# Performance work log

Measured on AMD Instinct MI355X. Metric: run time of the kernel, lower is better.

Reference implementation:

```python
import jax, jax.numpy as jnp
import numpy as np

B, T, D, H, DFF, E = 4, 1024, 1024, 16, 4096, 8
DH = D // H
EPS = 1e-6


def setup_inputs() -> dict:
    key = jax.random.key(0)
    ks = jax.random.split(key, 16)
    s = 0.02
    return {
        "x": jax.random.normal(ks[0], (B, T, D), jnp.float32),
        "mask": jnp.ones((B, 1, 1, T), jnp.bool_),
        "Wq": jax.random.normal(ks[1], (D, D), jnp.float32) * s,
        "bq": jnp.zeros((D,), jnp.float32),
        "Wk": jax.random.normal(ks[2], (D, D), jnp.float32) * s,
        "bk": jnp.zeros((D,), jnp.float32),
        "Wv": jax.random.normal(ks[3], (D, D), jnp.float32) * s,
        "bv": jnp.zeros((D,), jnp.float32),
        "Wo": jax.random.normal(ks[4], (D, D), jnp.float32) * s,
        "bo": jnp.zeros((D,), jnp.float32),
        "ln1_a": jnp.ones((D,), jnp.float32),
        "ln1_b": jnp.zeros((D,), jnp.float32),
        "ln2_a": jnp.ones((D,), jnp.float32),
        "ln2_b": jnp.zeros((D,), jnp.float32),
        "gW": jax.random.normal(ks[5], (D, E), jnp.float32) * s,
        "gb": jnp.zeros((E,), jnp.float32),
        "W1": jax.random.normal(ks[6], (E, D, DFF), jnp.float32) * s,
        "b1": jnp.zeros((E, DFF), jnp.float32),
        "W2": jax.random.normal(ks[7], (E, DFF, D), jnp.float32) * s,
        "b2": jnp.zeros((E, D), jnp.float32),
    }


def layer_norm(x, a, b):
    # Faithful to source: torch std is unbiased (ddof=1), divides by (std + eps)
    mean = jnp.mean(x, -1, keepdims=True)
    std = jnp.std(x, -1, keepdims=True, ddof=1)
    return a * (x - mean) / (std + EPS) + b


def mha(x, mask, Wq, bq, Wk, bk, Wv, bv, Wo, bo):
    def split(h):
        return h.reshape(B, T, H, DH).transpose(0, 2, 1, 3)  # [B,H,T,DH]
    q = split(x @ Wq + bq)
    k = split(x @ Wk + bk)
    v = split(x @ Wv + bv)
    scores = jnp.einsum("bhqd,bhkd->bhqk", q, k) / jnp.sqrt(jnp.float32(DH))
    scores = jnp.where(mask, scores, jnp.float32(-1e9))
    attn = jax.nn.softmax(scores, axis=-1)
    out = jnp.einsum("bhqk,bhkd->bhqd", attn, v)
    out = out.transpose(0, 2, 1, 3).reshape(B, T, D)
    return out @ Wo + bo


def moe(xf, gW, gb, W1, b1, W2, b2):
    # xf: [N, D] flat tokens; top-1 Switch routing
    gate_probs = jax.nn.softmax(xf @ gW + gb, axis=-1)  # [N, E]
    top1_idx = jnp.argmax(gate_probs, axis=-1)          # [N]
    top1_p = jnp.max(gate_probs, axis=-1)               # [N]
    out = jnp.zeros_like(xf)
    for e in range(E):  # fixed small structural loop over experts
        h = jax.nn.relu(xf @ W1[e] + b1[e])
        oe = h @ W2[e] + b2[e]
        sel = (top1_idx == e).astype(xf.dtype)
        out = out + (sel * top1_p)[:, None] * oe
    counts = jax.nn.one_hot(top1_idx, E, dtype=jnp.float32).sum(0)
    aux_loss = jnp.sum((counts / (B * T)) ** 2) * E
    return out, aux_loss


def reference(x, mask, Wq, bq, Wk, bk, Wv, bv, Wo, bo,
              ln1_a, ln1_b, ln2_a, ln2_b, gW, gb, W1, b1, W2, b2):
    # sublayer[0]: x + attn(norm(x))  (dropout=0, inference)
    x1 = x + mha(layer_norm(x, ln1_a, ln1_b), mask, Wq, bq, Wk, bk, Wv, bv, Wo, bo)
    # MoE applied to x1 directly (source calls feed_forward(x), not on the norm)
    ff_out, aux_loss = moe(x1.reshape(-1, D), gW, gb, W1, b1, W2, b2)
    # sublayer[1] with lambda _: ff_out  -> x1 + ff_out (norm computed but discarded)
    x2 = x1 + ff_out.reshape(B, T, D)
    return x2, aux_loss
```

## Files before the change

kernel.cpp:

```cpp
#include <hip/hip_runtime.h>

#define DEV __device__ __forceinline__

typedef unsigned short u16;
typedef __bf16 bf16x8 __attribute__((ext_vector_type(8)));
typedef float f32x4 __attribute__((ext_vector_type(4)));

static constexpr int Bn = 4, Tn = 1024, Dn = 1024, Hn = 16, DFFn = 4096, En = 8;
static constexpr int Nn = Bn * Tn;
static constexpr int MAXT2 = 24;
static constexpr int MAXT1 = 40;
static constexpr int HROWS = 6144;

static constexpr int MT2_E = 0, MT2_P0 = 24;
static constexpr int MT1_E = 48, MT1_P0 = 88;
static constexpr int MCNT = 128, MCUR = 136, MSEG = 144, MPERM = 152;

static constexpr size_t WQKVT_O = 0;
static constexpr size_t WOT_O   = WQKVT_O + 3ull * 1024 * 1024 * 2;
static constexpr size_t W12T_O  = WOT_O + 1ull * 1024 * 1024 * 2;
static constexpr size_t X1F_O   = W12T_O + 8ull * 1024 * 4096 * 2;
static constexpr size_t XN_O    = X1F_O + (size_t)Nn * Dn * 4;
static constexpr size_t Q_O     = XN_O + (size_t)Nn * Dn * 2;
static constexpr size_t K_O     = Q_O + (size_t)Nn * Dn * 2;
static constexpr size_t VT_O    = K_O + (size_t)Nn * Dn * 2;
static constexpr size_t X1B_O   = VT_O + (size_t)Nn * Dn * 2;
static constexpr size_t P3_O    = XN_O;
static constexpr size_t H_O     = X1B_O + (size_t)Nn * Dn * 2;
static constexpr size_t TOPP_O  = H_O + (size_t)HROWS * DFFn * 2;
static constexpr size_t TIDX_O  = TOPP_O + (size_t)Nn * 4;
static constexpr size_t META_O  = TIDX_O + (size_t)Nn * 4;

DEV u16 f2bf(float f) {
  union { float f; unsigned u; } v; v.f = f;
  unsigned r = v.u + 0x7fffu + ((v.u >> 16) & 1u);
  return (u16)(r >> 16);
}
DEV float bf2f(u16 x) {
  union { unsigned u; float f; } v; v.u = ((unsigned)x) << 16;
  return v.f;
}

DEV void gload16(const void* g, void* l) {
  __builtin_amdgcn_global_load_lds(
      (__attribute__((address_space(1))) void*)(void*)g,
      (__attribute__((address_space(3))) void*)l, 16, 0, 0);
}

DEV void sdecode64(int o, int& row, int& c) {
  row = o >> 7;
  c = ((o >> 4) & 7) ^ (row & 7);
}

DEV int aswz(int r, int c) { return c ^ (r & 7) ^ (((r >> 3) & 3) << 1); }

#define SBAR __builtin_amdgcn_sched_barrier(0)

__global__ __launch_bounds__(256) void tcast_kernel(
    const float* __restrict__ src, u16* __restrict__ dst,
    int R, int C, long srcBatch, long dstBatch) {
  __shared__ u16 tile[64][65];
  src += (long)blockIdx.z * srcBatch;
  dst += (long)blockIdx.z * dstBatch;
  int r0 = blockIdx.y * 64, c0 = blockIdx.x * 64;
  int tr = threadIdx.x >> 4;
  int tc = (threadIdx.x & 15) * 4;
#pragma unroll
  for (int i = 0; i < 4; i++) {
    int r = tr + i * 16;
    float4 v = *reinterpret_cast<const float4*>(&src[(long)(r0 + r) * C + c0 + tc]);
    tile[r][tc + 0] = f2bf(v.x); tile[r][tc + 1] = f2bf(v.y);
    tile[r][tc + 2] = f2bf(v.z); tile[r][tc + 3] = f2bf(v.w);
  }
  __syncthreads();
#pragma unroll
  for (int i = 0; i < 4; i++) {
    int r = tr + i * 16;
    ushort4 o;
    o.x = tile[tc + 0][r]; o.y = tile[tc + 1][r];
    o.z = tile[tc + 2][r]; o.w = tile[tc + 3][r];
    *reinterpret_cast<ushort4*>(&dst[(long)(c0 + r) * R + r0 + tc]) = o;
  }
}

__global__ __launch_bounds__(256) void ln_kernel(
    const float* __restrict__ x, const float* __restrict__ a,
    const float* __restrict__ b, u16* __restrict__ xn) {
  __shared__ float red[8];
  int row = blockIdx.x, tid = threadIdx.x;
  int lane = tid & 63, w = tid >> 6;
  float4 v = *reinterpret_cast<const float4*>(&x[(size_t)row * 1024 + tid * 4]);
  float s = v.x + v.y + v.z + v.w;
  float sq = v.x * v.x + v.y * v.y + v.z * v.z + v.w * v.w;
#pragma unroll
  for (int sh = 1; sh <= 32; sh <<= 1) { s += __shfl_xor(s, sh); sq += __shfl_xor(sq, sh); }
  if (lane == 0) { red[w] = s; red[4 + w] = sq; }
  __syncthreads();
  s = red[0] + red[1] + red[2] + red[3];
  sq = red[4] + red[5] + red[6] + red[7];
  float mean = s * (1.0f / 1024.0f);
  float var = (sq - s * mean) * (1.0f / 1023.0f);
  float inv = 1.0f / (sqrtf(var) + 1e-6f);
  float4 av = *reinterpret_cast<const float4*>(&a[tid * 4]);
  float4 bv = *reinterpret_cast<const float4*>(&b[tid * 4]);
  ushort4 o;
  o.x = f2bf(av.x * (v.x - mean) * inv + bv.x);
  o.y = f2bf(av.y * (v.y - mean) * inv + bv.y);
  o.z = f2bf(av.z * (v.z - mean) * inv + bv.z);
  o.w = f2bf(av.w * (v.w - mean) * inv + bv.w);
  *reinterpret_cast<ushort4*>(&xn[(size_t)row * 1024 + tid * 4]) = o;
}

#define RD_A8(dst, Abase_, q)                                               \
  _Pragma("unroll")                                                         \
  for (int mi = 0; mi < 4; mi++)                                            \
    _Pragma("unroll")                                                       \
    for (int kk = 0; kk < 2; kk++) {                                        \
      int row_ = wm * 128 + (q) * 64 + mi * 16 + rl15;                      \
      dst[mi * 2 + kk] = *reinterpret_cast<const bf16x8*>(                  \
          Abase_ + row_ * 128 + ((kk * 64 + cL * 16) ^ ((row_ & 7) << 4))); \
    }

#define RD_B4(dst, Bbase_, q)                                               \
  _Pragma("unroll")                                                         \
  for (int ni = 0; ni < 2; ni++)                                            \
    _Pragma("unroll")                                                       \
    for (int kk = 0; kk < 2; kk++) {                                        \
      int row_ = wn * 64 + (q) * 32 + ni * 16 + rl15;                       \
      dst[ni * 2 + kk] = *reinterpret_cast<const bf16x8*>(                  \
          Bbase_ + row_ * 128 + ((kk * 64 + cL * 16) ^ ((row_ & 7) << 4))); \
    }

#define MM16(Aq, Bq, asrc, bsrc)                                            \
  __builtin_amdgcn_s_setprio(1);                                            \
  _Pragma("unroll")                                                         \
  for (int mi = 0; mi < 4; mi++)                                            \
    _Pragma("unroll")                                                       \
    for (int ni = 0; ni < 2; ni++)                                          \
      _Pragma("unroll")                                                     \
      for (int kk = 0; kk < 2; kk++)                                        \
        acc[(Aq) * 4 + mi][(Bq) * 2 + ni] =                                 \
            __builtin_amdgcn_mfma_f32_16x16x32_bf16(                        \
                asrc[mi * 2 + kk], bsrc[ni * 2 + kk],                       \
                acc[(Aq) * 4 + mi][(Bq) * 2 + ni], 0, 0, 0);                \
  __builtin_amdgcn_s_setprio(0);

template <int MODE, int NG>
__global__ __launch_bounds__(512, 2) void gemm8_k(
    const u16* __restrict__ Ag, const u16* __restrict__ Bg,
    const float* __restrict__ f0, const float* __restrict__ f1,
    const float* __restrict__ f2, u16* __restrict__ ob0, u16* __restrict__ ob1,
    u16* __restrict__ ob2, const int* __restrict__ meta) {
  constexpr int NSUB = 16;
  constexpr int MT = (MODE == 0) ? 16 : MAXT2;
  constexpr int NT = (MODE == 0) ? 12 : 16;

  __shared__ u16 As[2][256 * 64];
  __shared__ u16 Bs[2][256 * 64];

  const int tid = threadIdx.x, lane = tid & 63, w = tid >> 6;
  const int wm = w >> 2, wn = w & 3;
  const int cL = lane >> 4, rl15 = lane & 15;

  constexpr int NWG = MT * NT;
  constexpr int q8 = NWG >> 3;
  int b = blockIdx.x;
  int lg = (b & 7) * q8 + (b >> 3);
  constexpr int PERG = MT * NG;
  int g = lg / PERG, rem = lg - g * PERG;
  int mt = rem / NG;
  int nt = g * NG + (rem - (rem / NG) * NG);

  int m0 = mt * 256, n0 = nt * 256;
  const u16* Bbase = Bg;
  int e = 0, cnt = 0, seg = 0, pos0 = 0;
  if constexpr (MODE == 2) {
    e = meta[MT2_E + mt];
    if (e < 0) return;
    cnt = meta[MCNT + e];
    seg = meta[MSEG + e];
    pos0 = meta[MT2_P0 + mt];
    Bbase = Bg + (size_t)e * 4096 * 1024;
  }

  const u16* gA[4];
  const u16* gB[4];
#pragma unroll
  for (int j = 0; j < 4; j++) {
    int row, c;
    sdecode64(j * 8192 + tid * 16, row, c);
    if constexpr (MODE == 2) {
      int pos = pos0 + row; if (pos >= cnt) pos = cnt - 1;
      int tok = meta[MPERM + seg + pos];
      gA[j] = Ag + (size_t)tok * 1024 + c * 8;
    } else {
      gA[j] = Ag + (size_t)(m0 + row) * 1024 + c * 8;
    }
    gB[j] = Bbase + (size_t)(n0 + row) * 1024 + c * 8;
  }

#define STAGE_SLOT(t, slot)                                                   \
  {                                                                           \
    int bi_ = (t) & 1;                                                        \
    if constexpr ((slot) == 0) {                                              \
      gload16(gA[0] + (t) * 64, &As[bi_][0 * 4096 + tid * 8]);                \
      gload16(gA[1] + (t) * 64, &As[bi_][1 * 4096 + tid * 8]);                \
    } else if constexpr ((slot) == 1) {                                       \
      gload16(gB[0] + (t) * 64, &Bs[bi_][0 * 4096 + tid * 8]);                \
      gload16(gB[1] + (t) * 64, &Bs[bi_][1 * 4096 + tid * 8]);                \
    } else if constexpr ((slot) == 2) {                                       \
      gload16(gA[2] + (t) * 64, &As[bi_][2 * 4096 + tid * 8]);                \
      gload16(gA[3] + (t) * 64, &As[bi_][3 * 4096 + tid * 8]);                \
    } else {                                                                  \
      gload16(gB[2] + (t) * 64, &Bs[bi_][2 * 4096 + tid * 8]);                \
      gload16(gB[3] + (t) * 64, &Bs[bi_][3 * 4096 + tid * 8]);                \
    }                                                                         \
  }

  f32x4 acc[8][4] = {};
  bf16x8 a0[8], a1[8], b0[4], b1[4];

  STAGE_SLOT(0, 0) STAGE_SLOT(0, 1) STAGE_SLOT(0, 2) STAGE_SLOT(0, 3)
  STAGE_SLOT(1, 0)
  asm volatile("s_waitcnt vmcnt(2)" ::: "memory");
  __builtin_amdgcn_s_barrier();

  for (int t = 0; t < NSUB; t++) {
    const char* Ab = reinterpret_cast<const char*>(&As[t & 1][0]);
    const char* Bb = reinterpret_cast<const char*>(&Bs[t & 1][0]);

    RD_A8(a0, Ab, 0)
    RD_B4(b0, Bb, 0)
    RD_A8(a1, Ab, 1)
    if (t + 1 < NSUB) STAGE_SLOT(t + 1, 1)
    SBAR; asm volatile("s_waitcnt lgkmcnt(8)" ::: "memory"); SBAR;
    MM16(0, 0, a0, b0)

    RD_B4(b1, Bb, 1)
    if (t + 1 < NSUB) STAGE_SLOT(t + 1, 2)
    SBAR; asm volatile("s_waitcnt lgkmcnt(4)" ::: "memory"); SBAR;
    MM16(1, 0, a1, b0)

    RD_A8(a0, Ab, 0)
    if (t + 1 < NSUB) STAGE_SLOT(t + 1, 3)
    SBAR; asm volatile("s_waitcnt lgkmcnt(8)" ::: "memory"); SBAR;
    MM16(1, 1, a1, b1)

    SBAR; asm volatile("s_waitcnt lgkmcnt(0)" ::: "memory"); SBAR;
    MM16(0, 1, a0, b1)

    if (t + 1 < NSUB) {
      __builtin_amdgcn_s_barrier();
      if (t + 2 < NSUB) {
        STAGE_SLOT(t + 2, 0)
        asm volatile("s_waitcnt vmcnt(2)" ::: "memory");
      } else {
        asm volatile("s_waitcnt vmcnt(0)" ::: "memory");
      }
      __builtin_amdgcn_s_barrier();
    }
  }

  const int cl = rl15, rl = cL;
  if constexpr (MODE == 0) {
    int third = n0 >> 10;
    const float* bias = (third == 0) ? f0 : (third == 1) ? f1 : f2;
    const float qs = (third == 0) ? 0.125f : 1.0f;
#pragma unroll
    for (int ni = 0; ni < 4; ni++) {
      int col = n0 + wn * 64 + ni * 16 + cl;
      int jj = col & 1023;
      float bb_ = bias[jj];
      int hh = jj >> 6, dd = jj & 63;
#pragma unroll
      for (int mi = 0; mi < 8; mi++) {
        int t0 = m0 + wm * 128 + mi * 16 + rl * 4;
        int b_ = t0 >> 10, tt = t0 & 1023;
        size_t bh = (size_t)(b_ * Hn + hh);
        if (third == 2) {
          ushort4 o4;
          o4.x = f2bf(acc[mi][ni][0] + bb_); o4.y = f2bf(acc[mi][ni][1] + bb_);
          o4.z = f2bf(acc[mi][ni][2] + bb_); o4.w = f2bf(acc[mi][ni][3] + bb_);
          *reinterpret_cast<ushort4*>(&ob2[(bh * 64 + dd) * 1024 + tt]) = o4;
        } else {
          u16* dst = (third == 0) ? ob0 : ob1;
#pragma unroll
          for (int r = 0; r < 4; r++)
            dst[(bh * 1024 + tt + r) * 64 + dd] = f2bf((acc[mi][ni][r] + bb_) * qs);
        }
      }
    }
  } else {
#pragma unroll
    for (int ni = 0; ni < 4; ni++) {
      int col = n0 + wn * 64 + ni * 16 + cl;
      float b1_ = f0[(size_t)e * 4096 + col];
#pragma unroll
      for (int mi = 0; mi < 8; mi++) {
        int pos = pos0 + wm * 128 + mi * 16 + rl * 4;
#pragma unroll
        for (int r = 0; r < 4; r++) {
          float v = acc[mi][ni][r] + b1_;
          v = v > 0.0f ? v : 0.0f;
          ob0[(size_t)(seg + pos + r) * 4096 + col] = f2bf(v);
        }
      }
    }
  }
}

template <int MODE, int BM, int NG, int KSPLIT>
__global__ __launch_bounds__(256, 3) void gemm3_k(
    const u16* __restrict__ Ag, const u16* __restrict__ Bg,
    const float* __restrict__ f0, const float* __restrict__ xres,
    float* __restrict__ x1f, u16* __restrict__ ob0,
    u16* __restrict__ pout, const int* __restrict__ meta) {
  constexpr int K = (MODE == 3) ? 4096 : 1024;
  constexpr int KS = K / KSPLIT;
  constexpr int NSUB = KS >> 6;
  constexpr int MT = (MODE == 1) ? (4096 / BM) : MAXT1;
  constexpr int NT = 8;
  constexpr int WR = BM / 2;
  constexpr int MI = WR / 16;
  constexpr int CA = BM / 32;

  __shared__ u16 As[BM * 64];
  __shared__ u16 Bs[128 * 64];

  const int tid = threadIdx.x, lane = tid & 63, w = tid >> 6;
  const int wm = w >> 1, wn = w & 1;
  const int cL = lane >> 4, rl15 = lane & 15;

  constexpr int NWG = MT * NT * KSPLIT;
  constexpr int q8 = NWG >> 3;
  int b = blockIdx.x;
  int lg = (b & 7) * q8 + (b >> 3);
  constexpr int PERG = KSPLIT * MT * NG;
  int g = lg / PERG, rem = lg - g * PERG;
  int s = rem / (MT * NG); rem -= s * (MT * NG);
  int mt = rem / NG;
  int nt = g * NG + (rem - (rem / NG) * NG);

  int m0 = mt * BM, n0 = nt * 128;
  const int k0 = s * KS;
  const u16* Abase = Ag;
  const u16* Bbase = Bg;
  int e = 0, seg = 0, pos0 = 0;
  if constexpr (MODE == 3) {
    e = meta[MT1_E + mt];
    if (e < 0) return;
    seg = meta[MSEG + e];
    pos0 = meta[MT1_P0 + mt];
    Bbase = Bg + (size_t)e * 4096 * 1024;
    Abase = Ag + (size_t)(seg + pos0) * 4096;
    m0 = 0;
  }

  const u16* gA[CA];
  const u16* gB[4];
#pragma unroll
  for (int j = 0; j < CA; j++) {
    int row, c;
    sdecode64(j * 4096 + tid * 16, row, c);
    gA[j] = Abase + (size_t)(m0 + row) * K + k0 + c * 8;
  }
#pragma unroll
  for (int j = 0; j < 4; j++) {
    int row, c;
    sdecode64(j * 4096 + tid * 16, row, c);
    gB[j] = Bbase + (size_t)(n0 + row) * K + k0 + c * 8;
  }

  auto STAGE = [&](int t) {
#pragma unroll
    for (int j = 0; j < CA; j++)
      gload16(gA[j] + t * 64, &As[j * 2048 + tid * 8]);
#pragma unroll
    for (int j = 0; j < 4; j++)
      gload16(gB[j] + t * 64, &Bs[j * 2048 + tid * 8]);
  };

  f32x4 acc[MI][4] = {};
  const char* Ab = reinterpret_cast<const char*>(&As[0]);
  const char* Bb = reinterpret_cast<const char*>(&Bs[0]);

  STAGE(0);
  for (int t = 0; t < NSUB; t++) {
    asm volatile("s_waitcnt vmcnt(0)" ::: "memory");
    __builtin_amdgcn_s_barrier();
#pragma unroll
    for (int ph = 0; ph < 2; ph++) {
      bf16x8 af[MI], bfr[4];
#pragma unroll
      for (int mi = 0; mi < MI; mi++) {
        int row = wm * WR + mi * 16 + rl15;
        af[mi] = *reinterpret_cast<const bf16x8*>(
            Ab + row * 128 + ((ph * 64 + cL * 16) ^ ((row & 7) << 4)));
      }
#pragma unroll
      for (int ni = 0; ni < 4; ni++) {
        int row = wn * 64 + ni * 16 + rl15;
        bfr[ni] = *reinterpret_cast<const bf16x8*>(
            Bb + row * 128 + ((ph * 64 + cL * 16) ^ ((row & 7) << 4)));
      }
#pragma unroll
      for (int mi = 0; mi < MI; mi++)
#pragma unroll
        for (int ni = 0; ni < 4; ni++)
          acc[mi][ni] = __builtin_amdgcn_mfma_f32_16x16x32_bf16(
              af[mi], bfr[ni], acc[mi][ni], 0, 0, 0);
    }
    __builtin_amdgcn_s_barrier();
    if (t + 1 < NSUB) STAGE(t + 1);
  }

  const int cl = rl15, rl = cL;
  if constexpr (MODE == 1) {
#pragma unroll
    for (int ni = 0; ni < 4; ni++) {
      int col = n0 + wn * 64 + ni * 16 + cl;
      float bo_ = f0[col];
#pragma unroll
      for (int mi = 0; mi < MI; mi++) {
        int row = m0 + wm * WR + mi * 16 + rl * 4;
#pragma unroll
        for (int r = 0; r < 4; r++) {
          size_t idx = (size_t)(row + r) * 1024 + col;
          float v = acc[mi][ni][r] + bo_ + xres[idx];
          x1f[idx] = v;
          ob0[idx] = f2bf(v);
        }
      }
    }
  } else {
#pragma unroll
    for (int ni = 0; ni < 4; ni++) {
      int col = n0 + wn * 64 + ni * 16 + cl;
#pragma unroll
      for (int mi = 0; mi < MI; mi++) {
        int pos = pos0 + wm * WR + mi * 16 + rl * 4;
#pragma unroll
        for (int r = 0; r < 4; r++)
          pout[((size_t)s * HROWS + seg + pos + r) * 1024 + col] = f2bf(acc[mi][ni][r]);
      }
    }
  }
}

__global__ __launch_bounds__(256) void reduce3_kernel(
    const u16* __restrict__ P3, const float* __restrict__ x1f,
    const float* __restrict__ topp, const float* __restrict__ b2,
    const int* __restrict__ meta, float* __restrict__ out) {
  int bidx = blockIdx.x;
  int tile = bidx >> 7, rowin = bidx & 127;
  int e = meta[MT1_E + tile];
  if (e < 0) return;
  int cnt = meta[MCNT + e], seg = meta[MSEG + e];
  int pos = meta[MT1_P0 + tile] + rowin;
  if (pos >= cnt) return;
  int tok = meta[MPERM + seg + pos];
  size_t prow = (size_t)(seg + pos) * 1024;
  float p = topp[tok];
  int c = threadIdx.x * 4;
  ushort4 u0 = *reinterpret_cast<const ushort4*>(&P3[prow + c]);
  ushort4 u1 = *reinterpret_cast<const ushort4*>(&P3[(size_t)HROWS * 1024 + prow + c]);
  float4 xr = *reinterpret_cast<const float4*>(&x1f[(size_t)tok * 1024 + c]);
  float4 bb = *reinterpret_cast<const float4*>(&b2[e * 1024 + c]);
  float4 o;
  o.x = xr.x + p * (bf2f(u0.x) + bf2f(u1.x) + bb.x);
  o.y = xr.y + p * (bf2f(u0.y) + bf2f(u1.y) + bb.y);
  o.z = xr.z + p * (bf2f(u0.z) + bf2f(u1.z) + bb.z);
  o.w = xr.w + p * (bf2f(u0.w) + bf2f(u1.w) + bb.w);
  *reinterpret_cast<float4*>(&out[(size_t)tok * 1024 + c]) = o;
}

__global__ __launch_bounds__(256, 4) void attn_kernel(
    const u16* __restrict__ q, const u16* __restrict__ k,
    const u16* __restrict__ vt, u16* __restrict__ attn) {
  __shared__ u16 Ks[2][64 * 64];
  __shared__ u16 Vs[2][64 * 64];
  const int tid = threadIdx.x, lane = tid & 63, w = tid >> 6;
  const int g = lane >> 4, l15 = lane & 15;

  int bb = blockIdx.x;
  int lg = (bb & 7) * 128 + (bb >> 3);
  const int bh = lg >> 4;
  const int qt = lg & 15;
  const size_t qkbase = (size_t)bh * Tn * 64;
  const size_t vtbase = (size_t)bh * 64 * Tn;
  const int qrow0 = qt * 64 + w * 16;

  bf16x8 qf[2];
  {
    const u16* qp = q + qkbase + (size_t)(qrow0 + l15) * 64 + g * 8;
    qf[0] = *reinterpret_cast<const bf16x8*>(qp);
    qf[1] = *reinterpret_cast<const bf16x8*>(qp + 32);
  }

  const u16* gk[2];
  const u16* gv[2];
#pragma unroll
  for (int j = 0; j < 2; j++) {
    int sidx = j * 256 + tid;
    int r = sidx >> 3, p = sidx & 7;
    int c = aswz(r, p);
    gk[j] = k + qkbase + (size_t)r * 64 + c * 8;
    gv[j] = vt + vtbase + (size_t)r * Tn + c * 8;
  }

  auto STAGE = [&](int t) {
    int buf = t & 1;
#pragma unroll
    for (int j = 0; j < 2; j++) {
      int sidx = j * 256 + tid;
      gload16(gk[j] + (size_t)t * 4096, &Ks[buf][sidx * 8]);
      gload16(gv[j] + (size_t)t * 64, &Vs[buf][sidx * 8]);
    }
  };

  f32x4 o[4] = {};
  float mrun = -1e30f, lsum = 0.0f;

  STAGE(0);
  for (int t = 0; t < 16; t++) {
    asm volatile("s_waitcnt vmcnt(0)" ::: "memory");
    __builtin_amdgcn_s_barrier();
    if (t + 1 < 16) STAGE(t + 1);

    const char* Kb = reinterpret_cast<const char*>(&Ks[t & 1][0]);
    const char* Vb = reinterpret_cast<const char*>(&Vs[t & 1][0]);

    f32x4 sk[2][2];
#pragma unroll
    for (int kb = 0; kb < 2; kb++)
#pragma unroll
      for (int m = 0; m < 2; m++) {
        f32x4 sa = {};
#pragma unroll
        for (int ph = 0; ph < 2; ph++) {
          int ksel = kb * 32 + (l15 >> 2) * 8 + m * 4 + (lane & 3);
          int pch = aswz(ksel, g + ph * 4);
          bf16x8 kf = *reinterpret_cast<const bf16x8*>(Kb + ksel * 128 + pch * 16);
          sa = __builtin_amdgcn_mfma_f32_16x16x32_bf16(kf, qf[ph], sa, 0, 0, 0);
        }
        sk[kb][m] = sa;
      }

    float mx = -1e30f;
#pragma unroll
    for (int kb = 0; kb < 2; kb++)
#pragma unroll
      for (int m = 0; m < 2; m++)
#pragma unroll
        for (int r = 0; r < 4; r++) mx = fmaxf(mx, sk[kb][m][r]);
    mx = fmaxf(mx, __shfl_xor(mx, 16));
    mx = fmaxf(mx, __shfl_xor(mx, 32));
    float mn = fmaxf(mrun, mx);
    float rsc = __expf(mrun - mn);
    mrun = mn;

    float pv[2][8];
    float ps = 0.0f;
#pragma unroll
    for (int kb = 0; kb < 2; kb++)
#pragma unroll
      for (int m = 0; m < 2; m++)
#pragma unroll
        for (int r = 0; r < 4; r++) {
          float pe = __expf(sk[kb][m][r] - mn);
          pv[kb][m * 4 + r] = pe;
          ps += pe;
        }
    ps += __shfl_xor(ps, 16);
    ps += __shfl_xor(ps, 32);
    lsum = lsum * rsc + ps;
#pragma unroll
    for (int nf = 0; nf < 4; nf++)
#pragma unroll
      for (int r = 0; r < 4; r++) o[nf][r] *= rsc;

    bf16x8 pf[2];
#pragma unroll
    for (int kb = 0; kb < 2; kb++)
#pragma unroll
      for (int j = 0; j < 8; j++) pf[kb][j] = (__bf16)pv[kb][j];

#pragma unroll
    for (int nf = 0; nf < 4; nf++) {
      int d = nf * 16 + l15;
#pragma unroll
      for (int kb = 0; kb < 2; kb++) {
        int pch = aswz(d, g + kb * 4);
        bf16x8 vf = *reinterpret_cast<const bf16x8*>(Vb + d * 128 + pch * 16);
        o[nf] = __builtin_amdgcn_mfma_f32_16x16x32_bf16(vf, pf[kb], o[nf], 0, 0, 0);
      }
    }
  }

  float inv = 1.0f / lsum;
  int b_ = bh >> 4, h_ = bh & 15;
  int tok = qrow0 + l15;
#pragma unroll
  for (int nf = 0; nf < 4; nf++)
#pragma unroll
    for (int r = 0; r < 4; r++) {
      int d = nf * 16 + g * 4 + r;
      attn[((size_t)(b_ * Tn + tok)) * 1024 + h_ * 64 + d] = f2bf(o[nf][r] * inv);
    }
}

__global__ __launch_bounds__(256) void gate_kernel(
    const float* __restrict__ x1f, const float* __restrict__ gW,
    const float* __restrict__ gb, float* __restrict__ topp,
    int* __restrict__ tidx, int* __restrict__ meta) {
  int lane = threadIdx.x & 63;
  int n = blockIdx.x * 4 + (threadIdx.x >> 6);
  float acc[8] = {};
  const float* xr = x1f + (size_t)n * 1024;
  for (int kk = 0; kk < 16; kk++) {
    int kcol = kk * 64 + lane;
    float xv = xr[kcol];
    float4 g0 = *reinterpret_cast<const float4*>(&gW[kcol * 8]);
    float4 g1 = *reinterpret_cast<const float4*>(&gW[kcol * 8 + 4]);
    acc[0] = fmaf(xv, g0.x, acc[0]); acc[1] = fmaf(xv, g0.y, acc[1]);
    acc[2] = fmaf(xv, g0.z, acc[2]); acc[3] = fmaf(xv, g0.w, acc[3]);
    acc[4] = fmaf(xv, g1.x, acc[4]); acc[5] = fmaf(xv, g1.y, acc[5]);
    acc[6] = fmaf(xv, g1.z, acc[6]); acc[7] = fmaf(xv, g1.w, acc[7]);
  }
#pragma unroll
  for (int e2 = 0; e2 < 8; e2++)
#pragma unroll
    for (int sh = 1; sh <= 32; sh <<= 1) acc[e2] += __shfl_xor(acc[e2], sh);
  if (lane == 0) {
    float best = -1e30f; int bi = 0;
#pragma unroll
    for (int e2 = 0; e2 < 8; e2++) {
      float lgt = acc[e2] + gb[e2];
      if (lgt > best) { best = lgt; bi = e2; }
    }
    float den = 0.0f;
#pragma unroll
    for (int e2 = 0; e2 < 8; e2++) den += __expf(acc[e2] + gb[e2] - best);
    topp[n] = 1.0f / den;
    tidx[n] = bi;
    atomicAdd(&meta[MCNT + bi], 1);
  }
}

__global__ void scan_kernel(int* meta, float* aux_out) {
  if (threadIdx.x == 0) {
    int sb = 0, t2 = 0, t1 = 0;
    float aux = 0.0f;
    for (int e2 = 0; e2 < 8; e2++) {
      meta[MSEG + e2] = sb;
      int c = meta[MCNT + e2];
      int n2 = (c + 255) >> 8;
      for (int i = 0; i < n2; i++) { meta[MT2_E + t2] = e2; meta[MT2_P0 + t2] = i * 256; t2++; }
      int n1 = (c + 127) >> 7;
      for (int i = 0; i < n1; i++) { meta[MT1_E + t1] = e2; meta[MT1_P0 + t1] = i * 128; t1++; }
      sb += n2 << 8;
      float fr = (float)c * (1.0f / 4096.0f);
      aux += fr * fr;
    }
    for (; t2 < MAXT2; t2++) { meta[MT2_E + t2] = -1; meta[MT2_P0 + t2] = 0; }
    for (; t1 < MAXT1; t1++) { meta[MT1_E + t1] = -1; meta[MT1_P0 + t1] = 0; }
    aux_out[0] = aux * 8.0f;
  }
}

__global__ __launch_bounds__(256) void scatter_kernel(const int* __restrict__ tidx, int* meta) {
  int n = blockIdx.x * 256 + threadIdx.x;
  int e2 = tidx[n];
  int pos = atomicAdd(&meta[MCUR + e2], 1);
  meta[MPERM + meta[MSEG + e2] + pos] = n;
}

extern "C" void kernel_launch(void* const* d_in, const int* in_sizes, int n_in,
                              void* d_out, int out_size, void* d_ws, size_t ws_size,
                              hipStream_t stream) {
  const float* x   = (const float*)d_in[0];
  const float* Wq  = (const float*)d_in[2];
  const float* bq  = (const float*)d_in[3];
  const float* Wk  = (const float*)d_in[4];
  const float* bk  = (const float*)d_in[5];
  const float* Wv  = (const float*)d_in[6];
  const float* bv  = (const float*)d_in[7];
  const float* Wo  = (const float*)d_in[8];
  const float* bo  = (const float*)d_in[9];
  const float* ln1a = (const float*)d_in[10];
  const float* ln1b = (const float*)d_in[11];
  const float* gW  = (const float*)d_in[14];
  const float* gb  = (const float*)d_in[15];
  const float* W1  = (const float*)d_in[16];
  const float* b1  = (const float*)d_in[17];
  const float* W2  = (const float*)d_in[18];
  const float* b2  = (const float*)d_in[19];
  float* out = (float*)d_out;
  char* ws = (char*)d_ws;

  u16* wqkvt = (u16*)(ws + WQKVT_O);
  u16* wot   = (u16*)(ws + WOT_O);
  u16* w12t  = (u16*)(ws + W12T_O);
  u16* xn    = (u16*)(ws + XN_O);
  u16* qb    = (u16*)(ws + Q_O);
  u16* kb    = (u16*)(ws + K_O);
  u16* vtb   = (u16*)(ws + VT_O);
  float* x1f = (float*)(ws + X1F_O);
  u16* x1b   = (u16*)(ws + X1B_O);
  u16* p3    = (u16*)(ws + P3_O);
  u16* hb    = (u16*)(ws + H_O);
  float* topp = (float*)(ws + TOPP_O);
  int* tidx  = (int*)(ws + TIDX_O);
  int* meta  = (int*)(ws + META_O);

  hipMemsetAsync(meta + MCNT, 0, 16 * sizeof(int), stream);

  tcast_kernel<<<dim3(16, 16, 1), 256, 0, stream>>>(Wq, wqkvt, 1024, 1024, 0, 0);
  tcast_kernel<<<dim3(16, 16, 1), 256, 0, stream>>>(Wk, wqkvt + 1024 * 1024, 1024, 1024, 0, 0);
  tcast_kernel<<<dim3(16, 16, 1), 256, 0, stream>>>(Wv, wqkvt + 2 * 1024 * 1024, 1024, 1024, 0, 0);
  tcast_kernel<<<dim3(16, 16, 1), 256, 0, stream>>>(Wo, wot, 1024, 1024, 0, 0);
  tcast_kernel<<<dim3(64, 16, 8), 256, 0, stream>>>(W1, w12t, 1024, 4096,
                                                    (long)1024 * 4096, (long)4096 * 1024);

  ln_kernel<<<4096, 256, 0, stream>>>(x, ln1a, ln1b, xn);
  gemm8_k<0, 4><<<192, 512, 0, stream>>>(xn, wqkvt, bq, bk, bv, qb, kb, vtb, meta);
  attn_kernel<<<1024, 256, 0, stream>>>(qb, kb, vtb, xn);
  gemm3_k<1, 64, 4, 1><<<512, 256, 0, stream>>>(xn, wot, bo, x, x1f, x1b, nullptr, meta);
  gate_kernel<<<1024, 256, 0, stream>>>(x1f, gW, gb, topp, tidx, meta);
  scan_kernel<<<1, 64, 0, stream>>>(meta, out + (size_t)Nn * Dn);
  scatter_kernel<<<16, 256, 0, stream>>>(tidx, meta);
  gemm8_k<2, 4><<<384, 512, 0, stream>>>(x1b, w12t, b1, nullptr, nullptr, hb, nullptr,
                                         nullptr, meta);
  tcast_kernel<<<dim3(16, 64, 8), 256, 0, stream>>>(W2, w12t, 4096, 1024,
                                                    (long)4096 * 1024, (long)1024 * 4096);
  gemm3_k<3, 128, 2, 2><<<640, 256, 0, stream>>>(hb, w12t, nullptr, nullptr, nullptr,
                                                 nullptr, p3, meta);
  reduce3_kernel<<<MAXT1 * 128, 256, 0, stream>>>(p3, x1f, topp, b2, meta, out);
}
```

Before: 415.7 us.

## Stage GEMM and attention epilogues through swizzled LDS for 16-byte coalesced stores

The QKV/FFN1 GEMM epilogue and the attention output epilogue now write their results into LDS with an XOR swizzle, then read them back as 8-element vectors. This turns scattered 2-byte global stores into 16-byte coalesced row stores, including the transposed V layout. It costs extra barriers, LDS traffic and reuse of the operand tile buffers, and it assumes the staging buffers are large enough and that the tile index variables (qt, w, tid) exist in scope.

Measured after the change: 415.3 us. Within noise of the previous version (-0.1%).

```diff
diff --git a/kernel.cpp b/kernel.cpp
--- a/kernel.cpp
+++ b/kernel.cpp
@@ -5,6 +5,7 @@
 typedef unsigned short u16;
 typedef __bf16 bf16x8 __attribute__((ext_vector_type(8)));
 typedef float f32x4 __attribute__((ext_vector_type(4)));
+typedef unsigned short us8 __attribute__((ext_vector_type(8)));
 
 static constexpr int Bn = 4, Tn = 1024, Dn = 1024, Hn = 16, DFFn = 4096, En = 8;
 static constexpr int Nn = Bn * Tn;
@@ -261,49 +262,91 @@
     }
   }
 
+  __syncthreads();
+  u16* T0 = &As[0][0];
+  u16* T1 = &Bs[0][0];
   const int cl = rl15, rl = cL;
-  if constexpr (MODE == 0) {
-    int third = n0 >> 10;
-    const float* bias = (third == 0) ? f0 : (third == 1) ? f1 : f2;
-    const float qs = (third == 0) ? 0.125f : 1.0f;
+  const int third = (MODE == 0) ? (n0 >> 10) : 0;
+  {
+    const float* bias;
+    float qs = 1.0f;
+    if constexpr (MODE == 0) {
+      bias = (third == 0) ? f0 : (third == 1) ? f1 : f2;
+      if (third == 0) qs = 0.125f;
+    } else {
+      bias = f0 + (size_t)e * 4096;
+    }
 #pragma unroll
     for (int ni = 0; ni < 4; ni++) {
-      int col = n0 + wn * 64 + ni * 16 + cl;
-      int jj = col & 1023;
-      float bb_ = bias[jj];
-      int hh = jj >> 6, dd = jj & 63;
+      int col = wn * 64 + ni * 16 + cl;
+      float bb_;
+      if constexpr (MODE == 0) bb_ = bias[(n0 & 1023) + col];
+      else bb_ = bias[n0 + col];
+      int colo = ((col >> 3) << 3) + (col & 7);
 #pragma unroll
       for (int mi = 0; mi < 8; mi++) {
-        int t0 = m0 + wm * 128 + mi * 16 + rl * 4;
-        int b_ = t0 >> 10, tt = t0 & 1023;
-        size_t bh = (size_t)(b_ * Hn + hh);
-        if (third == 2) {
-          ushort4 o4;
-          o4.x = f2bf(acc[mi][ni][0] + bb_); o4.y = f2bf(acc[mi][ni][1] + bb_);
-          o4.z = f2bf(acc[mi][ni][2] + bb_); o4.w = f2bf(acc[mi][ni][3] + bb_);
-          *reinterpret_cast<ushort4*>(&ob2[(bh * 64 + dd) * 1024 + tt]) = o4;
-        } else {
-          u16* dst = (third == 0) ? ob0 : ob1;
-#pragma unroll
-          for (int r = 0; r < 4; r++)
-            dst[(bh * 1024 + tt + r) * 64 + dd] = f2bf((acc[mi][ni][r] + bb_) * qs);
+        int rb = wm * 128 + mi * 16 + rl * 4;
+        u16* base = (rb < 128) ? T0 : T1;
+#pragma unroll
+        for (int r = 0; r < 4; r++) {
+          int row = rb + r;
+          float v = acc[mi][ni][r] + bb_;
+          if constexpr (MODE == 2) v = v > 0.0f ? v : 0.0f;
+          else v *= qs;
+          int off = ((row & 127) << 8) + ((((col >> 3) ^ ((row >> 3) & 7)) << 3) | (col & 7));
+          base[off] = f2bf(v);
         }
       }
     }
+  }
+  __syncthreads();
+
+  if constexpr (MODE == 2) {
+#pragma unroll
+    for (int p = 0; p < 16; p++) {
+      int idx = p * 512 + tid;
+      int row = idx >> 5, ch = idx & 31;
+      int pch = ch ^ ((row >> 3) & 7);
+      u16* base = (row < 128) ? T0 : T1;
+      us8 v = *reinterpret_cast<const us8*>(base + ((row & 127) << 8) + (pch << 3));
+      *reinterpret_cast<us8*>(&ob0[(size_t)(seg + pos0 + row) * 4096 + n0 + ch * 8]) = v;
+    }
   } else {
-#pragma unroll
-    for (int ni = 0; ni < 4; ni++) {
-      int col = n0 + wn * 64 + ni * 16 + cl;
-      float b1_ = f0[(size_t)e * 4096 + col];
-#pragma unroll
-      for (int mi = 0; mi < 8; mi++) {
-        int pos = pos0 + wm * 128 + mi * 16 + rl * 4;
-#pragma unroll
-        for (int r = 0; r < 4; r++) {
-          float v = acc[mi][ni][r] + b1_;
-          v = v > 0.0f ? v : 0.0f;
-          ob0[(size_t)(seg + pos + r) * 4096 + col] = f2bf(v);
+    int b_ = m0 >> 10;
+    int tt0 = m0 & 1023;
+    int hb0 = (n0 & 1023) >> 6;
+    if (third < 2) {
+      u16* dst = (third == 0) ? ob0 : ob1;
+#pragma unroll
+      for (int p = 0; p < 16; p++) {
+        int idx = p * 512 + tid;
+        int row = idx >> 5, ch = idx & 31;
+        int pch = ch ^ ((row >> 3) & 7);
+        u16* base = (row < 128) ? T0 : T1;
+        us8 v = *reinterpret_cast<const us8*>(base + ((row & 127) << 8) + (pch << 3));
+        int h = hb0 + (ch >> 3);
+        size_t addr = ((size_t)(b_ * 16 + h) * 1024 + tt0 + row) * 64 + (ch & 7) * 8;
+        *reinterpret_cast<us8*>(&dst[addr]) = v;
+      }
+    } else {
+#pragma unroll
+      for (int p = 0; p < 16; p++) {
+        int idx = p * 512 + tid;
+        int tblk = idx & 31;
+        int dcomb = idx >> 5;
+        int h = dcomb >> 6, dd = dcomb & 63;
+        int colo = h * 64 + dd;
+        us8 v;
+#pragma unroll
+        for (int j = 0; j < 8; j++) {
+          int row = tblk * 8 + j;
+          u16* base = (row < 128) ? T0 : T1;
+          int off = ((row & 127) << 8) +
+                    ((((colo >> 3) ^ ((row >> 3) & 7)) << 3) | (colo & 7));
+          v[j] = base[off];
         }
+        size_t addr = ((size_t)(b_ * 16 + hb0 + h) * 64 + dd) * 1024 + tt0 + tblk * 8;
+        *reinterpret_cast<us8*>(&ob2[addr]) = v;
       }
     }
   }
@@ -597,16 +640,29 @@
     }
   }
 
+  __syncthreads();
+  u16* T = &Ks[0][0];
   float inv = 1.0f / lsum;
+#pragma unroll
+  for (int nf = 0; nf < 4; nf++)
+#pragma unroll
+    for (int r = 0; r < 4; r++) {
+      int row = w * 16 + l15;
+      int d = nf * 16 + g * 4 + r;
+      int off = (row << 6) + ((((d >> 3) ^ (row & 7)) << 3) | (d & 7));
+      T[off] = f2bf(o[nf][r] * inv);
+    }
+  __syncthreads();
   int b_ = bh >> 4, h_ = bh & 15;
-  int tok = qrow0 + l15;
-#pragma unroll
-  for (int nf = 0; nf < 4; nf++)
-#pragma unroll
-    for (int r = 0; r < 4; r++) {
-      int d = nf * 16 + g * 4 + r;
-      attn[((size_t)(b_ * Tn + tok)) * 1024 + h_ * 64 + d] = f2bf(o[nf][r] * inv);
-    }
+#pragma unroll
+  for (int p = 0; p < 2; p++) {
+    int idx = p * 256 + tid;
+    int row = idx >> 3, ch = idx & 7;
+    int pch = ch ^ (row & 7);
+    us8 v = *reinterpret_cast<const us8*>(T + (row << 6) + (pch << 3));
+    *reinterpret_cast<us8*>(
+        &attn[((size_t)(b_ * Tn + qt * 64 + row)) * 1024 + h_ * 64 + ch * 8]) = v;
+  }
 }
 
 __global__ __launch_bounds__(256) void gate_kernel(
```
